# Kernel optimization log

Measured on AMD Instinct MI355X. Metric: run time of the kernel, lower is better.

The kernel has to match this reference:

```python
import jax, jax.numpy as jnp
import numpy as np

D_MODEL = 1024
NUM_HEADS = 16


def setup_inputs() -> dict:
    key = jax.random.key(0)
    ks = jax.random.split(key, 9)
    B, S, D = 4, 1024, D_MODEL
    scale = 1.0 / np.sqrt(D)
    inp = {
        "query": jax.random.normal(ks[0], (B, S, D), dtype=jnp.float32),
        "key": jax.random.normal(ks[1], (B, S, D), dtype=jnp.float32),
        "value": jax.random.normal(ks[2], (B, S, D), dtype=jnp.float32),
        # causal mask: 1 = attend, 0 = blocked (masked_fill where mask==0)
        "mask": jnp.tril(jnp.ones((S, S), dtype=jnp.int32))[None, None, :, :],
        "Wq": jax.random.normal(ks[3], (D, D), dtype=jnp.float32) * scale,
        "Wk": jax.random.normal(ks[4], (D, D), dtype=jnp.float32) * scale,
        "Wv": jax.random.normal(ks[5], (D, D), dtype=jnp.float32) * scale,
        "Wo": jax.random.normal(ks[6], (D, D), dtype=jnp.float32) * scale,
        "bo": jnp.zeros((D,), dtype=jnp.float32),
    }
    return inp


def reference(query, key, value, mask, Wq, Wk, Wv, Wo, bo):
    B, S, D = query.shape
    H = NUM_HEADS
    dk = D // H
    # torch Linear: y = x @ W.T  (bias=False for q/k/v)
    def proj(x, W):
        return (x @ W.T).reshape(B, S, H, dk).transpose(0, 2, 1, 3)  # [B,H,S,dk]

    Q = proj(query, Wq)
    K = proj(key, Wk)
    V = proj(value, Wv)

    scores = jnp.einsum("bhqd,bhkd->bhqk", Q, K) / jnp.sqrt(
        jnp.asarray(dk, dtype=jnp.float32)
    )
    scores = jnp.where(mask == 0, jnp.asarray(-1e9, scores.dtype), scores)
    attn = jax.nn.softmax(scores, axis=-1)
    out = jnp.einsum("bhqk,bhkd->bhqd", attn, V)  # [B,H,S,dk]
    out = out.transpose(0, 2, 1, 3).reshape(B, S, D)
    return out @ Wo.T + bo
```

## Files before the change

### kernel.cpp

```cpp
#include <hip/hip_runtime.h>

typedef __bf16 bf16x8 __attribute__((ext_vector_type(8)));
typedef short  s16x8  __attribute__((ext_vector_type(8)));
typedef float  f32x4  __attribute__((ext_vector_type(4)));
typedef float  f32x16 __attribute__((ext_vector_type(16)));
typedef unsigned int   u32x4 __attribute__((ext_vector_type(4)));
typedef unsigned short u16x4 __attribute__((ext_vector_type(4)));

#define NH   16
#define HD   64
#define SEQ  1024
#define DM   1024
#define NB   4
#define MTOT 4096

#define SCALE_L2E 0.1803368801111204f

__device__ __forceinline__ unsigned short f2bf(float f) {
    unsigned u = __builtin_bit_cast(unsigned, f);
    u += 0x7FFFu + ((u >> 16) & 1u);
    return (unsigned short)(u >> 16);
}

__device__ __forceinline__ s16x8 cvt8(f32x4 a, f32x4 b) {
    s16x8 r;
    r[0] = (short)f2bf(a[0]); r[1] = (short)f2bf(a[1]);
    r[2] = (short)f2bf(a[2]); r[3] = (short)f2bf(a[3]);
    r[4] = (short)f2bf(b[0]); r[5] = (short)f2bf(b[1]);
    r[6] = (short)f2bf(b[2]); r[7] = (short)f2bf(b[3]);
    return r;
}

__device__ __forceinline__ unsigned short bfbits(float x) {
    __bf16 h = (__bf16)x;
    return __builtin_bit_cast(unsigned short, h);
}
__device__ __forceinline__ float bf2f(unsigned short b) {
    unsigned u = (unsigned)b << 16;
    return __builtin_bit_cast(float, u);
}
__device__ __forceinline__ unsigned pk2(float a, float b) {
    return (unsigned)bfbits(a) | ((unsigned)bfbits(b) << 16);
}

__device__ __forceinline__ void gl16(const void* g, void* l) {
    __builtin_amdgcn_global_load_lds(
        (const __attribute__((address_space(1))) unsigned int*)g,
        (__attribute__((address_space(3))) unsigned int*)l, 16, 0, 0);
}

__device__ __forceinline__ bf16x8 ldfrag(const char* base, int row, int cb) {
    return __builtin_bit_cast(bf16x8,
        *(const s16x8*)(base + row * 128 + (cb ^ ((row & 7) << 4))));
}

__global__ __launch_bounds__(256)
void cvt_kernel(const float* __restrict__ q, const float* __restrict__ k,
                const float* __restrict__ v, const float* __restrict__ wq,
                const float* __restrict__ wk, const float* __restrict__ wv,
                const float* __restrict__ wo,
                unsigned short* __restrict__ dq, unsigned short* __restrict__ dk,
                unsigned short* __restrict__ dv, unsigned short* __restrict__ dwq,
                unsigned short* __restrict__ dwk, unsigned short* __restrict__ dwv,
                unsigned short* __restrict__ dwo)
{
    const int id = blockIdx.x;
    const float* s; unsigned short* d; int off; float scl = 1.0f;
    if (id < 6144) {
        const int t = id >> 11; off = id & 2047;
        s = (t == 0) ? q : (t == 1) ? k : v;
        d = (t == 0) ? dq : (t == 1) ? dk : dv;
    } else {
        const int w = (id - 6144) >> 9; off = (id - 6144) & 511;
        s = (w == 0) ? wq : (w == 1) ? wk : (w == 2) ? wv : wo;
        d = (w == 0) ? dwq : (w == 1) ? dwk : (w == 2) ? dwv : dwo;
        if (w == 0) scl = SCALE_L2E;
    }
    const int idx = off * 2048 + threadIdx.x * 8;
    const f32x4* sp = (const f32x4*)(s + idx);
    *(s16x8*)(d + idx) = cvt8(sp[0] * scl, sp[1] * scl);
}

__device__ __forceinline__ void stage_half(const unsigned short* __restrict__ src,
                                           int grow0, int k0, char* ldsdst, int tid)
{
    const int wv  = tid >> 6;
    const int row = tid >> 3;
    const int scx = ((tid & 7) * 16) ^ ((row & 7) << 4);
    gl16((const char*)(src + (size_t)(grow0 + row) * DM + k0) + scx,
         ldsdst + wv * 1024);
    gl16((const char*)(src + (size_t)(grow0 + 64 + row) * DM + k0) + scx,
         ldsdst + 8192 + wv * 1024);
}

__global__ __launch_bounds__(512, 2)
void proj_kernel(const unsigned short* __restrict__ Xq,
                 const unsigned short* __restrict__ Xk,
                 const unsigned short* __restrict__ Xv,
                 const unsigned short* __restrict__ Wq,
                 const unsigned short* __restrict__ Wk,
                 const unsigned short* __restrict__ Wv,
                 unsigned short* __restrict__ Qo, unsigned short* __restrict__ Ko,
                 unsigned short* __restrict__ VTo)
{
    __shared__ char smem[147456];

    const int bid = blockIdx.x;
    const int swz = (bid & 7) * 24 + (bid >> 3);
    const int which = swz >> 6;
    const int rem   = swz & 63;
    const int m0 = (rem >> 2) * 256, n0 = (rem & 3) * 256;

    const unsigned short* X = (which == 0) ? Xq : (which == 1) ? Xk : Xv;
    const unsigned short* W = (which == 0) ? Wq : (which == 1) ? Wk : Wv;

    const int tid = threadIdx.x, lane = tid & 63, wv = tid >> 6;
    const int wrB = (wv >> 2) * 128;
    const int wcB = (wv & 3) * 64;
    const int fr = lane & 15, hi = lane >> 4, r4 = hi * 4;

    f32x4 acc[8][4];
    #pragma unroll
    for (int i = 0; i < 8; ++i)
        #pragma unroll
        for (int j = 0; j < 4; ++j) acc[i][j] = (f32x4){0.f, 0.f, 0.f, 0.f};

    stage_half(X, m0,       0, smem +     0, tid);
    stage_half(X, m0 + 128, 0, smem + 16384, tid);
    stage_half(W, n0,       0, smem + 32768, tid);
    stage_half(W, n0 + 128, 0, smem + 49152, tid);

    for (int t = 0; t < 16; ++t) {
        const char* Abuf = smem + (t & 1) * 65536;
        const char* Bbuf = Abuf + 32768;
        char* nb = smem + ((t & 1) ^ 1) * 65536;
        const int kn = (t + 1) * 64;

        bf16x8 af[2][4], bf01[2][2], bf23[2][2];

        if (t < 15) {
            stage_half(X, m0, kn, nb, tid);
            asm volatile("s_waitcnt vmcnt(2)" ::: "memory");
        } else {
            asm volatile("s_waitcnt vmcnt(0)" ::: "memory");
        }
        __builtin_amdgcn_s_barrier();
        __builtin_amdgcn_sched_barrier(0);
        #pragma unroll
        for (int ks = 0; ks < 2; ++ks) {
            const int cb = ks * 64 + hi * 16;
            #pragma unroll
            for (int mt = 0; mt < 4; ++mt) af[ks][mt] = ldfrag(Abuf, wrB + mt * 16 + fr, cb);
            #pragma unroll
            for (int nt = 0; nt < 2; ++nt) bf01[ks][nt] = ldfrag(Bbuf, wcB + nt * 16 + fr, cb);
        }
        __builtin_amdgcn_s_setprio(1);
        #pragma unroll
        for (int ks = 0; ks < 2; ++ks)
            #pragma unroll
            for (int mt = 0; mt < 4; ++mt)
                #pragma unroll
                for (int nt = 0; nt < 2; ++nt)
                    acc[mt][nt] = __builtin_amdgcn_mfma_f32_16x16x32_bf16(
                        af[ks][mt], bf01[ks][nt], acc[mt][nt], 0, 0, 0);
        __builtin_amdgcn_s_setprio(0);

        __builtin_amdgcn_s_barrier();
        __builtin_amdgcn_sched_barrier(0);
        #pragma unroll
        for (int ks = 0; ks < 2; ++ks) {
            const int cb = ks * 64 + hi * 16;
            #pragma unroll
            for (int nt = 0; nt < 2; ++nt) bf23[ks][nt] = ldfrag(Bbuf, wcB + 32 + nt * 16 + fr, cb);
        }
        if (t < 15) stage_half(X, m0 + 128, kn, nb + 16384, tid);
        __builtin_amdgcn_s_setprio(1);
        #pragma unroll
        for (int ks = 0; ks < 2; ++ks)
            #pragma unroll
            for (int mt = 0; mt < 4; ++mt)
                #pragma unroll
                for (int nt = 0; nt < 2; ++nt)
                    acc[mt][nt + 2] = __builtin_amdgcn_mfma_f32_16x16x32_bf16(
                        af[ks][mt], bf23[ks][nt], acc[mt][nt + 2], 0, 0, 0);
        __builtin_amdgcn_s_setprio(0);

        __builtin_amdgcn_s_barrier();
        __builtin_amdgcn_sched_barrier(0);
        #pragma unroll
        for (int ks = 0; ks < 2; ++ks) {
            const int cb = ks * 64 + hi * 16;
            #pragma unroll
            for (int mt = 0; mt < 4; ++mt) af[ks][mt] = ldfrag(Abuf, wrB + 64 + mt * 16 + fr, cb);
        }
        if (t < 15) stage_half(W, n0, kn, nb + 32768, tid);
        __builtin_amdgcn_s_setprio(1);
        #pragma unroll
        for (int ks = 0; ks < 2; ++ks)
            #pragma unroll
            for (int mt = 0; mt < 4; ++mt)
                #pragma unroll
                for (int nt = 0; nt < 2; ++nt)
                    acc[mt + 4][nt] = __builtin_amdgcn_mfma_f32_16x16x32_bf16(
                        af[ks][mt], bf01[ks][nt], acc[mt + 4][nt], 0, 0, 0);
        __builtin_amdgcn_s_setprio(0);

        __builtin_amdgcn_s_barrier();
        __builtin_amdgcn_sched_barrier(0);
        if (t < 15) stage_half(W, n0 + 128, kn, nb + 49152, tid);
        __builtin_amdgcn_s_setprio(1);
        #pragma unroll
        for (int ks = 0; ks < 2; ++ks)
            #pragma unroll
            for (int mt = 0; mt < 4; ++mt)
                #pragma unroll
                for (int nt = 0; nt < 2; ++nt)
                    acc[mt + 4][nt + 2] = __builtin_amdgcn_mfma_f32_16x16x32_bf16(
                        af[ks][mt], bf23[ks][nt], acc[mt + 4][nt + 2], 0, 0, 0);
        __builtin_amdgcn_s_setprio(0);
    }

    __syncthreads();

    unsigned short* sE = (unsigned short*)(smem + wv * 18432);
    #pragma unroll
    for (int mt = 0; mt < 8; ++mt)
        #pragma unroll
        for (int nt = 0; nt < 4; ++nt)
            #pragma unroll
            for (int r = 0; r < 4; ++r) {
                const int row = mt * 16 + r4 + r;
                const int col = nt * 16 + fr;
                sE[row * 72 + (col ^ (((row >> 3) & 7) << 3))] = f2bf(acc[mt][nt][r]);
            }
    asm volatile("s_waitcnt lgkmcnt(0)" ::: "memory");

    const int hB    = (n0 + wcB) >> 6;
    const int sbase = m0 + wrB;
    const int bb    = sbase >> 10;
    const int srow0 = sbase & 1023;

    if (which < 2) {
        unsigned short* QK = ((which == 0) ? Qo : Ko)
            + (((size_t)(bb * NH + hB)) * SEQ + srow0) * HD;
        #pragma unroll
        for (int it = 0; it < 16; ++it) {
            const int idx = it * 64 + lane;
            const int row = idx >> 3, c = idx & 7;
            s16x8 v = *(const s16x8*)&sE[row * 72 + ((c ^ ((row >> 3) & 7)) * 8)];
            *(s16x8*)(QK + (size_t)row * HD + c * 8) = v;
        }
    } else {
        const int t0 = srow0 >> 6;
        unsigned short* VD = VTo + (size_t)(bb * NH + hB) * (SEQ * HD)
                                 + (size_t)t0 * 4096;
        #pragma unroll
        for (int it = 0; it < 16; ++it) {
            const int tt = it >> 3, r = it & 7;
            const int sb = tt * 64 + (r >> 1) * 16 + (lane >> 5) * 8;
            const int d  = (lane & 31) + (r & 1) * 32;
            s16x8 v;
            #pragma unroll
            for (int j = 0; j < 8; ++j) {
                const int row = sb + j;
                v[j] = (short)sE[row * 72 + (d ^ (((row >> 3) & 7) << 3))];
            }
            *(s16x8*)(VD + (size_t)(tt * 8 + r) * 512 + lane * 8) = v;
        }
    }
}

__global__ __launch_bounds__(512, 2)
void outproj_kernel(const unsigned short* __restrict__ A,
                    const unsigned short* __restrict__ Wo,
                    const float* __restrict__ bo,
                    float* __restrict__ Cout)
{
    const int bid = blockIdx.x;
    const int swz = (bid & 7) * 32 + (bid >> 3);
    const int m0 = (swz >> 3) * 128, n0 = (swz & 7) * 128;

    __shared__ char sA[2][16384];
    __shared__ char sB[2][16384];

    const int tid = threadIdx.x, lane = tid & 63, wv = tid >> 6;
    const int wr = (wv >> 1) * 32;
    const int wc = (wv & 1) * 64;
    const int fr = lane & 15, hi = lane >> 4, r4 = hi * 4;

    f32x4 acc[2][4];
    #pragma unroll
    for (int i = 0; i < 2; ++i)
        #pragma unroll
        for (int j = 0; j < 4; ++j) acc[i][j] = (f32x4){0.f, 0.f, 0.f, 0.f};

    stage_half(A,  m0, 0, sA[0], tid);
    stage_half(Wo, n0, 0, sB[0], tid);

    for (int kt = 0; kt < 16; ++kt) {
        const int cur = kt & 1;
        if (kt < 15) {
            stage_half(A,  m0, (kt + 1) * 64, sA[cur ^ 1], tid);
            stage_half(Wo, n0, (kt + 1) * 64, sB[cur ^ 1], tid);
            asm volatile("s_waitcnt vmcnt(4)" ::: "memory");
        } else {
            asm volatile("s_waitcnt vmcnt(0)" ::: "memory");
        }
        __builtin_amdgcn_s_barrier();
        __builtin_amdgcn_sched_barrier(0);
        #pragma unroll
        for (int ks = 0; ks < 2; ++ks) {
            const int cb = ks * 64 + hi * 16;
            bf16x8 af[2], bfm[4];
            #pragma unroll
            for (int mt = 0; mt < 2; ++mt)
                af[mt] = ldfrag(sA[cur], wr + mt * 16 + fr, cb);
            #pragma unroll
            for (int nt = 0; nt < 4; ++nt)
                bfm[nt] = ldfrag(sB[cur], wc + nt * 16 + fr, cb);
            #pragma unroll
            for (int mt = 0; mt < 2; ++mt)
                #pragma unroll
                for (int nt = 0; nt < 4; ++nt)
                    acc[mt][nt] = __builtin_amdgcn_mfma_f32_16x16x32_bf16(
                        af[mt], bfm[nt], acc[mt][nt], 0, 0, 0);
        }
        asm volatile("s_waitcnt lgkmcnt(0)" ::: "memory");
        __builtin_amdgcn_sched_barrier(0);
        __builtin_amdgcn_s_barrier();
    }

    #pragma unroll
    for (int mt = 0; mt < 2; ++mt)
        #pragma unroll
        for (int nt = 0; nt < 4; ++nt)
            #pragma unroll
            for (int r = 0; r < 4; ++r) {
                int gm = m0 + wr + mt * 16 + r4 + r;
                int gn = n0 + wc + nt * 16 + fr;
                Cout[(size_t)gm * DM + gn] = acc[mt][nt][r] + bo[gn];
            }
}

__device__ __forceinline__ void stageK64(const char* Kc, int t, char* myK, int lane) {
    const int krow8 = lane >> 3;
    const int kcol  = ((lane & 7) * 16) ^ (krow8 << 4);
    const char* kb = Kc + (size_t)t * 8192;
    #pragma unroll
    for (int i = 0; i < 8; ++i)
        gl16(kb + (i * 8 + krow8) * 128 + kcol, myK + i * 1024);
}

__global__ __launch_bounds__(256)
void attn_kernel(const unsigned short* __restrict__ Q,
                 const unsigned short* __restrict__ K,
                 const unsigned short* __restrict__ VT,
                 unsigned short* __restrict__ O)
{
    __shared__ char smem[4][8192];

    const int bid = blockIdx.x;
    const int xcd = bid & 7, idx = bid >> 3;
    const int bh  = xcd * 8 + (idx & 7);
    const int rb  = 15 - (idx >> 3);
    const int tid = threadIdx.x, lane = tid & 63, wv = tid >> 6;
    const int g = wv >> 1, p = wv & 1;
    const int q0w = rb * 64 + g * 32;
    const int ql = lane & 31, hi = lane >> 5;
    const int qg = q0w + ql;
    const int ndiag = q0w >> 6;

    char* myK = smem[wv];

    const unsigned short* Qp = Q + (size_t)bh * SEQ * HD;
    const char* Kc  = (const char*)(K  + (size_t)bh * SEQ * HD);
    const char* Vfc = (const char*)(VT + (size_t)bh * SEQ * HD);

    bf16x8 qf[4];
    #pragma unroll
    for (int s = 0; s < 4; ++s)
        qf[s] = __builtin_bit_cast(bf16x8,
            *(const s16x8*)(Qp + (size_t)qg * HD + s * 16 + hi * 8));

    f32x16 o0, o1;
    #pragma unroll
    for (int i = 0; i < 16; ++i) { o0[i] = 0.f; o1[i] = 0.f; }
    float mrow = -3.0e38f, lrow = 0.f;

    if (p <= ndiag) stageK64(Kc, p, myK, lane);

    for (int t = p; t <= ndiag; t += 2) {
        asm volatile("s_waitcnt vmcnt(0)" ::: "memory");
        __builtin_amdgcn_sched_barrier(0);

        f32x16 s0, s1;
        #pragma unroll
        for (int i = 0; i < 16; ++i) { s0[i] = 0.f; s1[i] = 0.f; }
        #pragma unroll
        for (int s = 0; s < 4; ++s) {
            const int cb = s * 32 + hi * 16;
            bf16x8 k0 = ldfrag(myK, ql, cb);
            bf16x8 k1 = ldfrag(myK, 32 + ql, cb);
            s0 = __builtin_amdgcn_mfma_f32_32x32x16_bf16(k0, qf[s], s0, 0, 0, 0);
            s1 = __builtin_amdgcn_mfma_f32_32x32x16_bf16(k1, qf[s], s1, 0, 0, 0);
        }
        asm volatile("s_waitcnt lgkmcnt(0)" ::: "memory");
        __builtin_amdgcn_sched_barrier(0);

        const char* vb = Vfc + (size_t)t * 8192;
        s16x8 vr[8];
        #pragma unroll
        for (int r = 0; r < 8; ++r)
            vr[r] = *(const s16x8*)(vb + r * 1024 + lane * 16);
        if (t + 2 <= ndiag) stageK64(Kc, t + 2, myK, lane);

        if (t == ndiag) {
            #pragma unroll
            for (int r = 0; r < 16; ++r) {
                const int kl = t * 64 + (r & 3) + 8 * (r >> 2) + 4 * hi;
                s0[r] = (kl      <= qg) ? s0[r] : -3.0e38f;
                s1[r] = (kl + 32 <= qg) ? s1[r] : -3.0e38f;
            }
        }

        float mt = s0[0];
        #pragma unroll
        for (int r = 1; r < 16; ++r) mt = fmaxf(mt, s0[r]);
        #pragma unroll
        for (int r = 0; r < 16; ++r) mt = fmaxf(mt, s1[r]);
        mt = fmaxf(mt, __shfl_xor(mt, 32, 64));

        if (!__all(mt - mrow <= 8.0f)) {
            const float mnew = fmaxf(mrow, mt);
            const float pc = __builtin_amdgcn_exp2f(mrow - mnew);
            mrow = mnew;
            lrow *= pc;
            #pragma unroll
            for (int i = 0; i < 16; ++i) { o0[i] *= pc; o1[i] *= pc; }
        }

        float ts = 0.f;
        #pragma unroll
        for (int r = 0; r < 16; ++r) { s0[r] = __builtin_amdgcn_exp2f(s0[r] - mrow); ts += s0[r]; }
        #pragma unroll
        for (int r = 0; r < 16; ++r) { s1[r] = __builtin_amdgcn_exp2f(s1[r] - mrow); ts += s1[r]; }
        ts += __shfl_xor(ts, 32, 64);
        lrow += ts;

        #pragma unroll
        for (int s = 0; s < 4; ++s) {
            const f32x16 ps = (s < 2) ? s0 : s1;
            const int bse = (s & 1) * 8;
            unsigned w0 = pk2(ps[bse + 0], ps[bse + 1]);
            unsigned w1 = pk2(ps[bse + 2], ps[bse + 3]);
            unsigned w2 = pk2(ps[bse + 4], ps[bse + 5]);
            unsigned w3 = pk2(ps[bse + 6], ps[bse + 7]);
            unsigned x0 = (unsigned)__shfl_xor((int)(hi ? w0 : w2), 32, 64);
            unsigned x1 = (unsigned)__shfl_xor((int)(hi ? w1 : w3), 32, 64);
            u32x4 fw;
            fw[0] = hi ? x0 : w0;
            fw[1] = hi ? x1 : w1;
            fw[2] = hi ? w2 : x0;
            fw[3] = hi ? w3 : x1;
            const bf16x8 pfrag = __builtin_bit_cast(bf16x8, fw);
            o0 = __builtin_amdgcn_mfma_f32_32x32x16_bf16(
                __builtin_bit_cast(bf16x8, vr[2 * s]), pfrag, o0, 0, 0, 0);
            o1 = __builtin_amdgcn_mfma_f32_32x32x16_bf16(
                __builtin_bit_cast(bf16x8, vr[2 * s + 1]), pfrag, o1, 0, 0, 0);
        }
    }

    if (p == 1) {
        unsigned* rec = (unsigned*)smem[wv] + lane * 21;
        #pragma unroll
        for (int i = 0; i < 8; ++i) rec[i]     = pk2(o0[2 * i], o0[2 * i + 1]);
        #pragma unroll
        for (int i = 0; i < 8; ++i) rec[8 + i] = pk2(o1[2 * i], o1[2 * i + 1]);
        rec[16] = __builtin_bit_cast(unsigned, mrow);
        rec[17] = __builtin_bit_cast(unsigned, lrow);
        asm volatile("s_waitcnt lgkmcnt(0)" ::: "memory");
    }
    __syncthreads();
    if (p == 0) {
        const unsigned* rec = (const unsigned*)smem[wv + 1] + lane * 21;
        const float m1 = __builtin_bit_cast(float, rec[16]);
        const float l1 = __builtin_bit_cast(float, rec[17]);
        const float ms = fmaxf(mrow, m1);
        const float c0 = __builtin_amdgcn_exp2f(mrow - ms);
        const float c1 = __builtin_amdgcn_exp2f(m1 - ms);
        const float inv = 1.0f / (lrow * c0 + l1 * c1);
        const float a0 = c0 * inv, a1 = c1 * inv;

        unsigned short* sE = (unsigned short*)smem[wv];
        #pragma unroll
        for (int dt = 0; dt < 2; ++dt) {
            const f32x16 ov = dt ? o1 : o0;
            #pragma unroll
            for (int j = 0; j < 4; ++j) {
                u16x4 w;
                #pragma unroll
                for (int i = 0; i < 4; ++i) {
                    const int ii = 4 * j + i;
                    const unsigned uw = rec[dt * 8 + (ii >> 1)];
                    const float pv = bf2f((unsigned short)((ii & 1) ? (uw >> 16) : (uw & 0xffff)));
                    w[i] = bfbits(ov[ii] * a0 + pv * a1);
                }
                *(u16x4*)&sE[ql * 72 + dt * 32 + 8 * j + 4 * hi] = w;
            }
        }
        asm volatile("s_waitcnt lgkmcnt(0)" ::: "memory");
        const int bb = bh >> 4, h = bh & 15;
        #pragma unroll
        for (int it = 0; it < 4; ++it) {
            const int ix = it * 64 + lane;
            const int qq = ix >> 3, c = ix & 7;
            s16x8 v = *(const s16x8*)&sE[qq * 72 + c * 8];
            *(s16x8*)(O + ((size_t)(bb * SEQ + q0w + qq) * DM + h * 64) + c * 8) = v;
        }
    }
}

extern "C" void kernel_launch(void* const* d_in, const int* in_sizes, int n_in,
                              void* d_out, int out_size, void* d_ws, size_t ws_size,
                              hipStream_t stream)
{
    const float* query = (const float*)d_in[0];
    const float* key   = (const float*)d_in[1];
    const float* value = (const float*)d_in[2];
    const float* Wq = (const float*)d_in[4];
    const float* Wk = (const float*)d_in[5];
    const float* Wv = (const float*)d_in[6];
    const float* Wo = (const float*)d_in[7];
    const float* bo = (const float*)d_in[8];
    float* out = (float*)d_out;

    const size_t XE = (size_t)MTOT * DM;
    const size_t WE = (size_t)DM * DM;
    unsigned short* ws16 = (unsigned short*)d_ws;
    unsigned short* Xq16 = ws16;
    unsigned short* Xk16 = Xq16 + XE;
    unsigned short* Xv16 = Xk16 + XE;
    unsigned short* Wq16 = Xv16 + XE;
    unsigned short* Wk16 = Wq16 + WE;
    unsigned short* Wv16 = Wk16 + WE;
    unsigned short* Wo16 = Wv16 + WE;
    unsigned short* Qw   = Wo16 + WE;
    unsigned short* Kw   = Qw + XE;
    unsigned short* VTw  = Kw + XE;
    unsigned short* AO   = VTw + XE;

    cvt_kernel<<<dim3(8192), dim3(256), 0, stream>>>(
        query, key, value, Wq, Wk, Wv, Wo,
        Xq16, Xk16, Xv16, Wq16, Wk16, Wv16, Wo16);

    proj_kernel<<<dim3(192), dim3(512), 0, stream>>>(
        Xq16, Xk16, Xv16, Wq16, Wk16, Wv16, Qw, Kw, VTw);

    attn_kernel<<<dim3(1024), dim3(256), 0, stream>>>(Qw, Kw, VTw, AO);

    outproj_kernel<<<dim3(256), dim3(512), 0, stream>>>(AO, Wo16, bo, out);
}
```

Before: 89.87 us.

## Process two 32-row query groups per wave to reuse K/V tiles

Each wave now handles 64 query rows as two 32-row groups, sharing each staged K tile and V register load between both groups, and the attention grid is halved. This cuts redundant K/V global and LDS traffic per query. In exchange it doubles accumulator and Q-fragment registers, which may lower occupancy, and it reduces the number of blocks. It also serializes the finalization across two barrier rounds.

Result: slower. 96.99 us (+7.9%).

```diff
diff --git a/kernel.cpp b/kernel.cpp
--- a/kernel.cpp
+++ b/kernel.cpp
@@ -362,13 +362,15 @@
     const int bid = blockIdx.x;
     const int xcd = bid & 7, idx = bid >> 3;
     const int bh  = xcd * 8 + (idx & 7);
-    const int rb  = 15 - (idx >> 3);
+    const int blkgrp = idx >> 3;
     const int tid = threadIdx.x, lane = tid & 63, wv = tid >> 6;
-    const int g = wv >> 1, p = wv & 1;
-    const int q0w = rb * 64 + g * 32;
+    const int rb  = 15 - (blkgrp * 2 + (wv >> 1));
+    const int p   = wv & 1;
+    const int q0  = rb * 64;
     const int ql = lane & 31, hi = lane >> 5;
-    const int qg = q0w + ql;
-    const int ndiag = q0w >> 6;
+    const int qga = q0 + ql;
+    const int qgb = q0 + 32 + ql;
+    const int ndiag = rb;
 
     char* myK = smem[wv];
 
@@ -376,18 +378,21 @@
     const char* Kc  = (const char*)(K  + (size_t)bh * SEQ * HD);
     const char* Vfc = (const char*)(VT + (size_t)bh * SEQ * HD);
 
-    bf16x8 qf[4];
-    #pragma unroll
-    for (int s = 0; s < 4; ++s)
-        qf[s] = __builtin_bit_cast(bf16x8,
-            *(const s16x8*)(Qp + (size_t)qg * HD + s * 16 + hi * 8));
-
-    f32x16 o0, o1;
-    #pragma unroll
-    for (int i = 0; i < 16; ++i) { o0[i] = 0.f; o1[i] = 0.f; }
-    float mrow = -3.0e38f, lrow = 0.f;
-
-    if (p <= ndiag) stageK64(Kc, p, myK, lane);
+    bf16x8 qfa[4], qfb[4];
+    #pragma unroll
+    for (int s = 0; s < 4; ++s) {
+        qfa[s] = __builtin_bit_cast(bf16x8,
+            *(const s16x8*)(Qp + (size_t)qga * HD + s * 16 + hi * 8));
+        qfb[s] = __builtin_bit_cast(bf16x8,
+            *(const s16x8*)(Qp + (size_t)qgb * HD + s * 16 + hi * 8));
+    }
+
+    f32x16 o0a, o1a, o0b, o1b;
+    #pragma unroll
+    for (int i = 0; i < 16; ++i) { o0a[i] = 0.f; o1a[i] = 0.f; o0b[i] = 0.f; o1b[i] = 0.f; }
+    float mra = -3.0e38f, lra = 0.f, mrb = -3.0e38f, lrb = 0.f;
+
+    stageK64(Kc, p, myK, lane);
 
     for (int t = p; t <= ndiag; t += 2) {
         asm volatile("s_waitcnt vmcnt(0)" ::: "memory");
@@ -401,8 +406,8 @@
             const int cb = s * 32 + hi * 16;
             bf16x8 k0 = ldfrag(myK, ql, cb);
             bf16x8 k1 = ldfrag(myK, 32 + ql, cb);
-            s0 = __builtin_amdgcn_mfma_f32_32x32x16_bf16(k0, qf[s], s0, 0, 0, 0);
-            s1 = __builtin_amdgcn_mfma_f32_32x32x16_bf16(k1, qf[s], s1, 0, 0, 0);
+            s0 = __builtin_amdgcn_mfma_f32_32x32x16_bf16(k0, qfa[s], s0, 0, 0, 0);
+            s1 = __builtin_amdgcn_mfma_f32_32x32x16_bf16(k1, qfa[s], s1, 0, 0, 0);
         }
         asm volatile("s_waitcnt lgkmcnt(0)" ::: "memory");
         __builtin_amdgcn_sched_barrier(0);
@@ -412,40 +417,39 @@
         #pragma unroll
         for (int r = 0; r < 8; ++r)
             vr[r] = *(const s16x8*)(vb + r * 1024 + lane * 16);
-        if (t + 2 <= ndiag) stageK64(Kc, t + 2, myK, lane);
 
         if (t == ndiag) {
             #pragma unroll
             for (int r = 0; r < 16; ++r) {
                 const int kl = t * 64 + (r & 3) + 8 * (r >> 2) + 4 * hi;
-                s0[r] = (kl      <= qg) ? s0[r] : -3.0e38f;
-                s1[r] = (kl + 32 <= qg) ? s1[r] : -3.0e38f;
-            }
-        }
-
-        float mt = s0[0];
-        #pragma unroll
-        for (int r = 1; r < 16; ++r) mt = fmaxf(mt, s0[r]);
-        #pragma unroll
-        for (int r = 0; r < 16; ++r) mt = fmaxf(mt, s1[r]);
-        mt = fmaxf(mt, __shfl_xor(mt, 32, 64));
-
-        if (!__all(mt - mrow <= 8.0f)) {
-            const float mnew = fmaxf(mrow, mt);
-            const float pc = __builtin_amdgcn_exp2f(mrow - mnew);
-            mrow = mnew;
-            lrow *= pc;
-            #pragma unroll
-            for (int i = 0; i < 16; ++i) { o0[i] *= pc; o1[i] *= pc; }
-        }
-
-        float ts = 0.f;
-        #pragma unroll
-        for (int r = 0; r < 16; ++r) { s0[r] = __builtin_amdgcn_exp2f(s0[r] - mrow); ts += s0[r]; }
-        #pragma unroll
-        for (int r = 0; r < 16; ++r) { s1[r] = __builtin_amdgcn_exp2f(s1[r] - mrow); ts += s1[r]; }
-        ts += __shfl_xor(ts, 32, 64);
-        lrow += ts;
+                s0[r] = (kl      <= qga) ? s0[r] : -3.0e38f;
+                s1[r] = (kl + 32 <= qga) ? s1[r] : -3.0e38f;
+            }
+        }
+
+        {
+            float mt = s0[0];
+            #pragma unroll
+            for (int r = 1; r < 16; ++r) mt = fmaxf(mt, s0[r]);
+            #pragma unroll
+            for (int r = 0; r < 16; ++r) mt = fmaxf(mt, s1[r]);
+            mt = fmaxf(mt, __shfl_xor(mt, 32, 64));
+            if (!__all(mt - mra <= 8.0f)) {
+                const float mnew = fmaxf(mra, mt);
+                const float pc = __builtin_amdgcn_exp2f(mra - mnew);
+                mra = mnew;
+                lra *= pc;
+                #pragma unroll
+                for (int i = 0; i < 16; ++i) { o0a[i] *= pc; o1a[i] *= pc; }
+            }
+            float ts = 0.f;
+            #pragma unroll
+            for (int r = 0; r < 16; ++r) { s0[r] = __builtin_amdgcn_exp2f(s0[r] - mra); ts += s0[r]; }
+            #pragma unroll
+            for (int r = 0; r < 16; ++r) { s1[r] = __builtin_amdgcn_exp2f(s1[r] - mra); ts += s1[r]; }
+            ts += __shfl_xor(ts, 32, 64);
+            lra += ts;
+        }
 
         #pragma unroll
         for (int s = 0; s < 4; ++s) {
@@ -463,60 +467,140 @@
             fw[2] = hi ? w2 : x0;
             fw[3] = hi ? w3 : x1;
             const bf16x8 pfrag = __builtin_bit_cast(bf16x8, fw);
-            o0 = __builtin_amdgcn_mfma_f32_32x32x16_bf16(
-                __builtin_bit_cast(bf16x8, vr[2 * s]), pfrag, o0, 0, 0, 0);
-            o1 = __builtin_amdgcn_mfma_f32_32x32x16_bf16(
-                __builtin_bit_cast(bf16x8, vr[2 * s + 1]), pfrag, o1, 0, 0, 0);
+            o0a = __builtin_amdgcn_mfma_f32_32x32x16_bf16(
+                __builtin_bit_cast(bf16x8, vr[2 * s]), pfrag, o0a, 0, 0, 0);
+            o1a = __builtin_amdgcn_mfma_f32_32x32x16_bf16(
+                __builtin_bit_cast(bf16x8, vr[2 * s + 1]), pfrag, o1a, 0, 0, 0);
+        }
+
+        #pragma unroll
+        for (int i = 0; i < 16; ++i) { s0[i] = 0.f; s1[i] = 0.f; }
+        #pragma unroll
+        for (int s = 0; s < 4; ++s) {
+            const int cb = s * 32 + hi * 16;
+            bf16x8 k0 = ldfrag(myK, ql, cb);
+            bf16x8 k1 = ldfrag(myK, 32 + ql, cb);
+            s0 = __builtin_amdgcn_mfma_f32_32x32x16_bf16(k0, qfb[s], s0, 0, 0, 0);
+            s1 = __builtin_amdgcn_mfma_f32_32x32x16_bf16(k1, qfb[s], s1, 0, 0, 0);
+        }
+        asm volatile("s_waitcnt lgkmcnt(0)" ::: "memory");
+        __builtin_amdgcn_sched_barrier(0);
+
+        if (t + 2 <= ndiag) stageK64(Kc, t + 2, myK, lane);
+
+        if (t == ndiag) {
+            #pragma unroll
+            for (int r = 0; r < 16; ++r) {
+                const int kl = t * 64 + (r & 3) + 8 * (r >> 2) + 4 * hi;
+                s0[r] = (kl      <= qgb) ? s0[r] : -3.0e38f;
+                s1[r] = (kl + 32 <= qgb) ? s1[r] : -3.0e38f;
+            }
+        }
+
+        {
+            float mt = s0[0];
+            #pragma unroll
+            for (int r = 1; r < 16; ++r) mt = fmaxf(mt, s0[r]);
+            #pragma unroll
+            for (int r = 0; r < 16; ++r) mt = fmaxf(mt, s1[r]);
+            mt = fmaxf(mt, __shfl_xor(mt, 32, 64));
+            if (!__all(mt - mrb <= 8.0f)) {
+                const float mnew = fmaxf(mrb, mt);
+                const float pc = __builtin_amdgcn_exp2f(mrb - mnew);
+                mrb = mnew;
+                lrb *= pc;
+                #pragma unroll
+                for (int i = 0; i < 16; ++i) { o0b[i] *= pc; o1b[i] *= pc; }
+            }
+            float ts = 0.f;
+            #pragma unroll
+            for (int r = 0; r < 16; ++r) { s0[r] = __builtin_amdgcn_exp2f(s0[r] - mrb); ts += s0[r]; }
+            #pragma unroll
+            for (int r = 0; r < 16; ++r) { s1[r] = __builtin_amdgcn_exp2f(s1[r] - mrb); ts += s1[r]; }
+            ts += __shfl_xor(ts, 32, 64);
+            lrb += ts;
+        }
+
+        #pragma unroll
+        for (int s = 0; s < 4; ++s) {
+            const f32x16 ps = (s < 2) ? s0 : s1;
+            const int bse = (s & 1) * 8;
+            unsigned w0 = pk2(ps[bse + 0], ps[bse + 1]);
+            unsigned w1 = pk2(ps[bse + 2], ps[bse + 3]);
+            unsigned w2 = pk2(ps[bse + 4], ps[bse + 5]);
+            unsigned w3 = pk2(ps[bse + 6], ps[bse + 7]);
+            unsigned x0 = (unsigned)__shfl_xor((int)(hi ? w0 : w2), 32, 64);
+            unsigned x1 = (unsigned)__shfl_xor((int)(hi ? w1 : w3), 32, 64);
+            u32x4 fw;
+            fw[0] = hi ? x0 : w0;
+            fw[1] = hi ? x1 : w1;
+            fw[2] = hi ? w2 : x0;
+            fw[3] = hi ? w3 : x1;
+            const bf16x8 pfrag = __builtin_bit_cast(bf16x8, fw);
+            o0b = __builtin_amdgcn_mfma_f32_32x32x16_bf16(
+                __builtin_bit_cast(bf16x8, vr[2 * s]), pfrag, o0b, 0, 0, 0);
+            o1b = __builtin_amdgcn_mfma_f32_32x32x16_bf16(
+                __builtin_bit_cast(bf16x8, vr[2 * s + 1]), pfrag, o1b, 0, 0, 0);
         }
     }
 
-    if (p == 1) {
-        unsigned* rec = (unsigned*)smem[wv] + lane * 21;
-        #pragma unroll
-        for (int i = 0; i < 8; ++i) rec[i]     = pk2(o0[2 * i], o0[2 * i + 1]);
-        #pragma unroll
-        for (int i = 0; i < 8; ++i) rec[8 + i] = pk2(o1[2 * i], o1[2 * i + 1]);
-        rec[16] = __builtin_bit_cast(unsigned, mrow);
-        rec[17] = __builtin_bit_cast(unsigned, lrow);
-        asm volatile("s_waitcnt lgkmcnt(0)" ::: "memory");
-    }
-    __syncthreads();
-    if (p == 0) {
-        const unsigned* rec = (const unsigned*)smem[wv + 1] + lane * 21;
-        const float m1 = __builtin_bit_cast(float, rec[16]);
-        const float l1 = __builtin_bit_cast(float, rec[17]);
-        const float ms = fmaxf(mrow, m1);
-        const float c0 = __builtin_amdgcn_exp2f(mrow - ms);
-        const float c1 = __builtin_amdgcn_exp2f(m1 - ms);
-        const float inv = 1.0f / (lrow * c0 + l1 * c1);
-        const float a0 = c0 * inv, a1 = c1 * inv;
-
-        unsigned short* sE = (unsigned short*)smem[wv];
-        #pragma unroll
-        for (int dt = 0; dt < 2; ++dt) {
-            const f32x16 ov = dt ? o1 : o0;
-            #pragma unroll
-            for (int j = 0; j < 4; ++j) {
-                u16x4 w;
-                #pragma unroll
-                for (int i = 0; i < 4; ++i) {
-                    const int ii = 4 * j + i;
-                    const unsigned uw = rec[dt * 8 + (ii >> 1)];
-                    const float pv = bf2f((unsigned short)((ii & 1) ? (uw >> 16) : (uw & 0xffff)));
-                    w[i] = bfbits(ov[ii] * a0 + pv * a1);
+    const int bb = bh >> 4, h = bh & 15;
+    #pragma unroll
+    for (int gsel = 0; gsel < 2; ++gsel) {
+        const f32x16 po0 = gsel ? o0b : o0a;
+        const f32x16 po1 = gsel ? o1b : o1a;
+        const float  pm  = gsel ? mrb : mra;
+        const float  pl  = gsel ? lrb : lra;
+        const int    qrow0 = q0 + gsel * 32;
+
+        if (p == 1) {
+            unsigned* rec = (unsigned*)smem[wv] + lane * 21;
+            #pragma unroll
+            for (int i = 0; i < 8; ++i) rec[i]     = pk2(po0[2 * i], po0[2 * i + 1]);
+            #pragma unroll
+            for (int i = 0; i < 8; ++i) rec[8 + i] = pk2(po1[2 * i], po1[2 * i + 1]);
+            rec[16] = __builtin_bit_cast(unsigned, pm);
+            rec[17] = __builtin_bit_cast(unsigned, pl);
+            asm volatile("s_waitcnt lgkmcnt(0)" ::: "memory");
+        }
+        __syncthreads();
+        if (p == 0) {
+            const unsigned* rec = (const unsigned*)smem[wv + 1] + lane * 21;
+            const float m1 = __builtin_bit_cast(float, rec[16]);
+            const float l1 = __builtin_bit_cast(float, rec[17]);
+            const float ms = fmaxf(pm, m1);
+            const float c0 = __builtin_amdgcn_exp2f(pm - ms);
+            const float c1 = __builtin_amdgcn_exp2f(m1 - ms);
+            const float inv = 1.0f / (pl * c0 + l1 * c1);
+            const float a0 = c0 * inv, a1 = c1 * inv;
+
+            unsigned short* sE = (unsigned short*)smem[wv];
+            #pragma unroll
+            for (int dt = 0; dt < 2; ++dt) {
+                const f32x16 ov = dt ? po1 : po0;
+                #pragma unroll
+                for (int j = 0; j < 4; ++j) {
+                    u16x4 w;
+                    #pragma unroll
+                    for (int i = 0; i < 4; ++i) {
+                        const int ii = 4 * j + i;
+                        const unsigned uw = rec[dt * 8 + (ii >> 1)];
+                        const float pv = bf2f((unsigned short)((ii & 1) ? (uw >> 16) : (uw & 0xffff)));
+                        w[i] = bfbits(ov[ii] * a0 + pv * a1);
+                    }
+                    *(u16x4*)&sE[ql * 72 + dt * 32 + 8 * j + 4 * hi] = w;
                 }
-                *(u16x4*)&sE[ql * 72 + dt * 32 + 8 * j + 4 * hi] = w;
-            }
-        }
-        asm volatile("s_waitcnt lgkmcnt(0)" ::: "memory");
-        const int bb = bh >> 4, h = bh & 15;
-        #pragma unroll
-        for (int it = 0; it < 4; ++it) {
-            const int ix = it * 64 + lane;
-            const int qq = ix >> 3, c = ix & 7;
-            s16x8 v = *(const s16x8*)&sE[qq * 72 + c * 8];
-            *(s16x8*)(O + ((size_t)(bb * SEQ + q0w + qq) * DM + h * 64) + c * 8) = v;
-        }
+            }
+            asm volatile("s_waitcnt lgkmcnt(0)" ::: "memory");
+            #pragma unroll
+            for (int it = 0; it < 4; ++it) {
+                const int ix = it * 64 + lane;
+                const int qq = ix >> 3, c = ix & 7;
+                s16x8 v = *(const s16x8*)&sE[qq * 72 + c * 8];
+                *(s16x8*)(O + ((size_t)(bb * SEQ + qrow0 + qq) * DM + h * 64) + c * 8) = v;
+            }
+        }
+        __syncthreads();
     }
 }
 
@@ -556,7 +640,7 @@
     proj_kernel<<<dim3(192), dim3(512), 0, stream>>>(
         Xq16, Xk16, Xv16, Wq16, Wk16, Wv16, Qw, Kw, VTw);
 
-    attn_kernel<<<dim3(1024), dim3(256), 0, stream>>>(Qw, Kw, VTw, AO);
+    attn_kernel<<<dim3(512), dim3(256), 0, stream>>>(Qw, Kw, VTw, AO);
 
     outproj_kernel<<<dim3(256), dim3(512), 0, stream>>>(AO, Wo16, bo, out);
 }
```
